# Performance work log

Hardware: AMD Instinct MI355X
Metric: run time of the kernel (lower is better)

The kernel has to match this reference:

```python
import jax, jax.numpy as jnp
import numpy as np

OUT, IN, GROUP = 8192, 8192, 128  # meta.shape=(out,in), group_size over out dim


def unpack_int4(packed, out_shape):
    """Unpack uint8 bytes (two nibbles each) into signed int8 in [-8,7].
    Matches torch: inter[0::2]=lo, inter[1::2]=hi."""
    flat = packed.reshape(-1)
    lo = (flat & 15).astype(jnp.int8)
    hi = ((flat >> 4) & 15).astype(jnp.int8)
    lo = jnp.where(lo >= 8, lo - 16, lo)
    hi = jnp.where(hi >= 8, hi - 16, hi)
    inter = jnp.stack([lo, hi], axis=-1).reshape(-1)  # interleave lo/hi
    total = out_shape[0] * out_shape[1]
    return inter[:total].reshape(out_shape)


def setup_inputs() -> dict:
    key = jax.random.key(0)
    kx, kq, ks, kb = jax.random.split(key, 4)
    x = jax.random.normal(kx, (16, IN), dtype=jnp.float32)
    # packed int4 weights: one byte holds two nibbles -> OUT*IN/2 bytes
    q_packed = jax.random.randint(kq, (OUT * IN // 2,), 0, 256, dtype=jnp.int32).astype(jnp.uint8)
    # per-group scales (group over out dim), positive small values
    scale = jax.random.uniform(ks, (OUT // GROUP,), dtype=jnp.float32) * 0.01 + 1e-4
    bias = jax.random.normal(kb, (OUT,), dtype=jnp.float32) * 0.01
    return {"x": x, "q_packed": q_packed, "scale": scale, "bias": bias}


def reference(x, q_packed, scale, bias):
    # unpack + per-group dequant, then matmul (CPU fallback path of QuantLinear.forward)
    q_int = unpack_int4(q_packed, (OUT, IN)).astype(jnp.float32)  # (OUT, IN)
    s = jnp.repeat(scale, GROUP)[:, None]                         # (OUT, 1) expanded scales
    W = s * q_int                                                 # dequantized fp weight
    return x @ W.T + bias                                         # (B, OUT)
```

## Files before the change

kernel.cpp:

```cpp
#include <hip/hip_runtime.h>
#include <hip/hip_bf16.h>

#define OUT_N 8192
#define IN_N  8192
#define QROW  (IN_N / 2)
#define NCH   8
#define CH32  64

typedef __attribute__((ext_vector_type(8))) short short8v;
typedef __attribute__((ext_vector_type(4))) float f32x4;

__device__ __forceinline__ unsigned int bf16pk(float a, float b) {
    __hip_bfloat162 h = __float22bfloat162_rn(make_float2(a, b));
    unsigned int u;
    __builtin_memcpy(&u, &h, 4);
    return u;
}

__device__ __forceinline__ void gld_lds16(const int* gsrc, int* ldst_base) {
    __builtin_amdgcn_global_load_lds(
        (const __attribute__((address_space(1))) void*)gsrc,
        (__attribute__((address_space(3))) void*)ldst_base, 16, 0, 0);
}

__global__ __launch_bounds__(256) void xconv_kernel(
    const float* __restrict__ x, uint4* __restrict__ xb2)
{
    const int tid = blockIdx.x * 256 + threadIdx.x;
    const int l   = tid & 63;
    const int scs = tid >> 6;
    const int s   = scs & 3;
    const int c   = (scs >> 2) & 7;
    const int w   = scs >> 5;
    const int r   = l & 15;
    const int g   = l >> 4;
    const float* src = x + (size_t)r * IN_N + w * 1024 + c * 128 + s * 32 + g * 8;
    float4 a = *(const float4*)src;
    float4 b = *(const float4*)(src + 4);
    uint4 u = { bf16pk(a.x, a.y), bf16pk(a.z, a.w),
                bf16pk(b.x, b.y), bf16pk(b.z, b.w) };
    xb2[tid] = u;
}

__global__ __launch_bounds__(512, 4) void qlin_mfma_kernel(
    const int*   __restrict__ qp,
    const uint4* __restrict__ xb2,
    const float* __restrict__ scale,
    const float* __restrict__ bias,
    float*       __restrict__ out)
{
    __shared__ int   qbuf[8][2][16 * CH32];
    __shared__ float red[8][16][17];

    const int t = threadIdx.x;
    const int w = t >> 6;
    const int l = t & 63;
    const int g = l >> 4;
    const int r = l & 15;
    const int tile = blockIdx.x;
    const int obase = tile * 16;
    const int ph = tile & 7;

    const int* qwbase = qp + (size_t)obase * QROW + w * (QROW / 8);
    const int drow = l >> 4;
    const uint4* xwbase = xb2 + (w << 11) + l;

    f32x4 acc = {0.f, 0.f, 0.f, 0.f};
    uint4 xr[2][4];

    #pragma unroll
    for (int s = 0; s < 4; ++s)
        xr[0][s] = xwbase[ph * 256 + s * 64];
    #pragma unroll
    for (int p = 0; p < 4; ++p) {
        const int row = 4 * p + drow;
        const int j   = (l & 15) ^ (row & 15);
        gld_lds16(qwbase + (size_t)row * QROW + ph * CH32 + j * 4,
                  &qbuf[w][0][p * 256]);
    }

    #pragma unroll
    for (int c0 = 0; c0 < NCH; ++c0) {
        const int cur = c0 & 1;

        if (c0 + 1 < NCH) {
            const int ccn = (c0 + 1 + ph) & 7;
            #pragma unroll
            for (int s = 0; s < 4; ++s)
                xr[cur ^ 1][s] = xwbase[ccn * 256 + s * 64];
            #pragma unroll
            for (int p = 0; p < 4; ++p) {
                const int row = 4 * p + drow;
                const int j   = (l & 15) ^ (row & 15);
                gld_lds16(qwbase + (size_t)row * QROW + ccn * CH32 + j * 4,
                          &qbuf[w][cur ^ 1][p * 256]);
            }
            asm volatile("s_waitcnt vmcnt(8)" ::: "memory");
        } else {
            asm volatile("s_waitcnt vmcnt(0)" ::: "memory");
        }
        __builtin_amdgcn_sched_barrier(0);

        const char* wb = (const char*)qbuf[w][cur];
        #pragma unroll
        for (int s = 0; s < 4; ++s) {
            const int4 q = *(const int4*)(wb + r * 256 + ((((s << 2) + g) ^ r) << 4));
            uint4 ub = {
                bf16pk((float)((q.x << 28) >> 28), (float)((q.x << 24) >> 28)),
                bf16pk((float)((q.y << 28) >> 28), (float)((q.y << 24) >> 28)),
                bf16pk((float)((q.z << 28) >> 28), (float)((q.z << 24) >> 28)),
                bf16pk((float)((q.w << 28) >> 28), (float)((q.w << 24) >> 28))
            };
            short8v bfrag = __builtin_bit_cast(short8v, ub);
            short8v afrag = __builtin_bit_cast(short8v, xr[cur][s]);
            acc = __builtin_amdgcn_mfma_f32_16x16x32_bf16(afrag, bfrag, acc, 0, 0, 0);
        }
    }

    red[w][g * 4 + 0][r] = acc[0];
    red[w][g * 4 + 1][r] = acc[1];
    red[w][g * 4 + 2][r] = acc[2];
    red[w][g * 4 + 3][r] = acc[3];
    __syncthreads();

    if (t < 256) {
        const int b = t >> 4;
        const int o = t & 15;
        const int oc = obase + o;
        float v = 0.f;
        #pragma unroll
        for (int i = 0; i < 8; ++i) v += red[i][b][o];
        out[b * OUT_N + oc] = v * scale[oc >> 7] + bias[oc];
    }
}

extern "C" void kernel_launch(void* const* d_in, const int* in_sizes, int n_in,
                              void* d_out, int out_size, void* d_ws, size_t ws_size,
                              hipStream_t stream) {
    (void)in_sizes; (void)n_in; (void)ws_size; (void)out_size;
    const float* x     = (const float*)d_in[0];
    const int*   qp    = (const int*)d_in[1];
    const float* scale = (const float*)d_in[2];
    const float* bias  = (const float*)d_in[3];
    float*       out   = (float*)d_out;
    uint4*       xb2   = (uint4*)d_ws;

    xconv_kernel<<<dim3(64), dim3(256), 0, stream>>>(x, xb2);
    qlin_mfma_kernel<<<dim3(OUT_N / 16), dim3(512), 0, stream>>>(qp, xb2, scale, bias, out);
}
```

Before: 30.79 us.

## Split block into producer DMA waves and consumer MFMA waves with LDS flags

Restructures the GEMV kernel so four waves only issue global-to-LDS loads of the int4 weight tile in 16 super-chunks, while four other waves dequantize and run MFMA, synchronizing through LDS flag arrays with spin-waits. The x conversion layout is reordered to match the new per-consumer-wave K split. The aim is to keep more weight loads in flight, decoupled from compute. The cost is spin-wait overhead on volatile LDS flags, half the waves doing no math, and a risk of ordering or visibility problems between the producer's DMA completion and the consumers' reads.

Result: slower. 40.14 us (+30.4%).

```diff
diff --git a/kernel.cpp b/kernel.cpp
--- a/kernel.cpp
+++ b/kernel.cpp
@@ -4,8 +4,8 @@
 #define OUT_N 8192
 #define IN_N  8192
 #define QROW  (IN_N / 2)
-#define NCH   8
-#define CH32  64
+#define NSC   16
+#define SC32  256
 
 typedef __attribute__((ext_vector_type(8))) short short8v;
 typedef __attribute__((ext_vector_type(4))) float f32x4;
@@ -23,18 +23,20 @@
         (__attribute__((address_space(3))) void*)ldst_base, 16, 0, 0);
 }
 
+#define SCHED0() __builtin_amdgcn_sched_barrier(0)
+#define CFENCE() asm volatile("" ::: "memory")
+
 __global__ __launch_bounds__(256) void xconv_kernel(
     const float* __restrict__ x, uint4* __restrict__ xb2)
 {
     const int tid = blockIdx.x * 256 + threadIdx.x;
-    const int l   = tid & 63;
-    const int scs = tid >> 6;
-    const int s   = scs & 3;
-    const int c   = (scs >> 2) & 7;
-    const int w   = scs >> 5;
-    const int r   = l & 15;
-    const int g   = l >> 4;
-    const float* src = x + (size_t)r * IN_N + w * 1024 + c * 128 + s * 32 + g * 8;
+    const int l  = tid & 63;
+    const int s  = (tid >> 6) & 3;
+    const int S  = (tid >> 8) & 15;
+    const int cw = tid >> 12;
+    const int r  = l & 15;
+    const int g  = l >> 4;
+    const float* src = x + (size_t)r * IN_N + S * 512 + cw * 128 + s * 32 + g * 8;
     float4 a = *(const float4*)src;
     float4 b = *(const float4*)(src + 4);
     uint4 u = { bf16pk(a.x, a.y), bf16pk(a.z, a.w),
@@ -42,15 +44,17 @@
     xb2[tid] = u;
 }
 
-__global__ __launch_bounds__(512, 4) void qlin_mfma_kernel(
+__global__ __launch_bounds__(512, 4) void qlin_pc_kernel(
     const int*   __restrict__ qp,
     const uint4* __restrict__ xb2,
     const float* __restrict__ scale,
     const float* __restrict__ bias,
     float*       __restrict__ out)
 {
-    __shared__ int   qbuf[8][2][16 * CH32];
-    __shared__ float red[8][16][17];
+    __shared__ int   qbuf[2][16][SC32];
+    __shared__ float red[4][16][17];
+    __shared__ int   psync[NSC][4];
+    __shared__ int   pdone[NSC][4];
 
     const int t = threadIdx.x;
     const int w = t >> 6;
@@ -59,77 +63,90 @@
     const int r = l & 15;
     const int tile = blockIdx.x;
     const int obase = tile * 16;
-    const int ph = tile & 7;
 
-    const int* qwbase = qp + (size_t)obase * QROW + w * (QROW / 8);
-    const int drow = l >> 4;
-    const uint4* xwbase = xb2 + (w << 11) + l;
+    if (t < NSC * 4) { ((int*)psync)[t] = 0; ((int*)pdone)[t] = 0; }
+    __syncthreads();
 
-    f32x4 acc = {0.f, 0.f, 0.f, 0.f};
-    uint4 xr[2][4];
+    if (w < 4) {
+        const int p = w;
+#define PDMA(S_) do { _Pragma("unroll")                                      \
+        for (int i = 0; i < 4; ++i) {                                        \
+            const int R = 4 * p + i;                                         \
+            gld_lds16(qp + (size_t)(obase + R) * QROW + (S_) * SC32          \
+                         + ((l ^ (R & 15)) << 2),                            \
+                      &qbuf[(S_) & 1][R][0]);                                \
+        } } while (0)
 
-    #pragma unroll
-    for (int s = 0; s < 4; ++s)
-        xr[0][s] = xwbase[ph * 256 + s * 64];
-    #pragma unroll
-    for (int p = 0; p < 4; ++p) {
-        const int row = 4 * p + drow;
-        const int j   = (l & 15) ^ (row & 15);
-        gld_lds16(qwbase + (size_t)row * QROW + ph * CH32 + j * 4,
-                  &qbuf[w][0][p * 256]);
+        PDMA(0);
+        PDMA(1);
+        #pragma unroll
+        for (int S = 0; S < NSC; ++S) {
+            if (S + 1 < NSC) asm volatile("s_waitcnt vmcnt(4)" ::: "memory");
+            else             asm volatile("s_waitcnt vmcnt(0)" ::: "memory");
+            SCHED0();
+            if (l == 0) psync[S][p] = 1;
+            if (S + 2 < NSC) {
+                volatile int* dn = &pdone[S][0];
+                while ((dn[0] & dn[1] & dn[2] & dn[3]) == 0)
+                    asm volatile("s_sleep 1");
+                CFENCE(); SCHED0();
+                PDMA(S + 2);
+            }
+        }
+#undef PDMA
+    } else {
+        const int cw = w - 4;
+        f32x4 acc = {0.f, 0.f, 0.f, 0.f};
+        const uint4* xbase = xb2 + cw * 4096 + l;
+
+        #pragma unroll
+        for (int S = 0; S < NSC; ++S) {
+            uint4 xr0 = xbase[S * 256 +   0];
+            uint4 xr1 = xbase[S * 256 +  64];
+            uint4 xr2 = xbase[S * 256 + 128];
+            uint4 xr3 = xbase[S * 256 + 192];
+            volatile int* sy = &psync[S][0];
+            while ((sy[0] & sy[1] & sy[2] & sy[3]) == 0)
+                asm volatile("s_sleep 1");
+            CFENCE(); SCHED0();
+            asm volatile("s_waitcnt vmcnt(0)" ::: "memory");
+            SCHED0();
+
+            const char* wb = (const char*)&qbuf[S & 1][0][0];
+            #pragma unroll
+            for (int s = 0; s < 4; ++s) {
+                const int slot = cw * 16 + s * 4 + g;
+                const int4 q = *(const int4*)(wb + r * 1024
+                                              + ((slot ^ (r & 15)) << 4));
+                uint4 ub = {
+                    bf16pk((float)((q.x << 28) >> 28), (float)((q.x << 24) >> 28)),
+                    bf16pk((float)((q.y << 28) >> 28), (float)((q.y << 24) >> 28)),
+                    bf16pk((float)((q.z << 28) >> 28), (float)((q.z << 24) >> 28)),
+                    bf16pk((float)((q.w << 28) >> 28), (float)((q.w << 24) >> 28))
+                };
+                short8v bfrag = __builtin_bit_cast(short8v, ub);
+                uint4 xcur = (s == 0) ? xr0 : (s == 1) ? xr1 : (s == 2) ? xr2 : xr3;
+                short8v afrag = __builtin_bit_cast(short8v, xcur);
+                acc = __builtin_amdgcn_mfma_f32_16x16x32_bf16(afrag, bfrag, acc, 0, 0, 0);
+            }
+            asm volatile("s_waitcnt lgkmcnt(0)" ::: "memory");
+            SCHED0();
+            if (l == 0) pdone[S][cw] = 1;
+        }
+
+        red[cw][g * 4 + 0][r] = acc[0];
+        red[cw][g * 4 + 1][r] = acc[1];
+        red[cw][g * 4 + 2][r] = acc[2];
+        red[cw][g * 4 + 3][r] = acc[3];
     }
 
-    #pragma unroll
-    for (int c0 = 0; c0 < NCH; ++c0) {
-        const int cur = c0 & 1;
-
-        if (c0 + 1 < NCH) {
-            const int ccn = (c0 + 1 + ph) & 7;
-            #pragma unroll
-            for (int s = 0; s < 4; ++s)
-                xr[cur ^ 1][s] = xwbase[ccn * 256 + s * 64];
-            #pragma unroll
-            for (int p = 0; p < 4; ++p) {
-                const int row = 4 * p + drow;
-                const int j   = (l & 15) ^ (row & 15);
-                gld_lds16(qwbase + (size_t)row * QROW + ccn * CH32 + j * 4,
-                          &qbuf[w][cur ^ 1][p * 256]);
-            }
-            asm volatile("s_waitcnt vmcnt(8)" ::: "memory");
-        } else {
-            asm volatile("s_waitcnt vmcnt(0)" ::: "memory");
-        }
-        __builtin_amdgcn_sched_barrier(0);
-
-        const char* wb = (const char*)qbuf[w][cur];
-        #pragma unroll
-        for (int s = 0; s < 4; ++s) {
-            const int4 q = *(const int4*)(wb + r * 256 + ((((s << 2) + g) ^ r) << 4));
-            uint4 ub = {
-                bf16pk((float)((q.x << 28) >> 28), (float)((q.x << 24) >> 28)),
-                bf16pk((float)((q.y << 28) >> 28), (float)((q.y << 24) >> 28)),
-                bf16pk((float)((q.z << 28) >> 28), (float)((q.z << 24) >> 28)),
-                bf16pk((float)((q.w << 28) >> 28), (float)((q.w << 24) >> 28))
-            };
-            short8v bfrag = __builtin_bit_cast(short8v, ub);
-            short8v afrag = __builtin_bit_cast(short8v, xr[cur][s]);
-            acc = __builtin_amdgcn_mfma_f32_16x16x32_bf16(afrag, bfrag, acc, 0, 0, 0);
-        }
-    }
-
-    red[w][g * 4 + 0][r] = acc[0];
-    red[w][g * 4 + 1][r] = acc[1];
-    red[w][g * 4 + 2][r] = acc[2];
-    red[w][g * 4 + 3][r] = acc[3];
     __syncthreads();
 
     if (t < 256) {
         const int b = t >> 4;
         const int o = t & 15;
         const int oc = obase + o;
-        float v = 0.f;
-        #pragma unroll
-        for (int i = 0; i < 8; ++i) v += red[i][b][o];
+        float v = red[0][b][o] + red[1][b][o] + red[2][b][o] + red[3][b][o];
         out[b * OUT_N + oc] = v * scale[oc >> 7] + bias[oc];
     }
 }
@@ -146,5 +163,5 @@
     uint4*       xb2   = (uint4*)d_ws;
 
     xconv_kernel<<<dim3(64), dim3(256), 0, stream>>>(x, xb2);
-    qlin_mfma_kernel<<<dim3(OUT_N / 16), dim3(512), 0, stream>>>(qp, xb2, scale, bias, out);
+    qlin_pc_kernel<<<dim3(OUT_N / 16), dim3(512), 0, stream>>>(qp, xb2, scale, bias, out);
 }
```

## Replace direct global-to-LDS loads with register-staged loads and deeper prefetch

Applied to the files above, without the earlier changes.

Weight chunks are now loaded from global memory into registers and then written to LDS by the threads, instead of using the global_load_lds direct path. The pipeline is restructured to prefetch two chunks ahead, storing the next chunk to LDS after the current MFMA work. The aim is to keep more memory requests in flight and overlap them with compute. The cost is more registers, extra LDS write instructions, and fragile hand-tuned vmcnt waits that have to match the new load ordering.

Measured after the change: 57.05 us. +85.3%, slower.

```diff
diff --git a/kernel.cpp b/kernel.cpp
--- a/kernel.cpp
+++ b/kernel.cpp
@@ -17,11 +17,7 @@
     return u;
 }
 
-__device__ __forceinline__ void gld_lds16(const int* gsrc, int* ldst_base) {
-    __builtin_amdgcn_global_load_lds(
-        (const __attribute__((address_space(1))) void*)gsrc,
-        (__attribute__((address_space(3))) void*)ldst_base, 16, 0, 0);
-}
+#define SCHED0() __builtin_amdgcn_sched_barrier(0)
 
 __global__ __launch_bounds__(256) void xconv_kernel(
     const float* __restrict__ x, uint4* __restrict__ xb2)
@@ -66,40 +62,40 @@
     const uint4* xwbase = xb2 + (w << 11) + l;
 
     f32x4 acc = {0.f, 0.f, 0.f, 0.f};
+    int4  qr[2][4];
     uint4 xr[2][4];
 
-    #pragma unroll
-    for (int s = 0; s < 4; ++s)
-        xr[0][s] = xwbase[ph * 256 + s * 64];
-    #pragma unroll
-    for (int p = 0; p < 4; ++p) {
-        const int row = 4 * p + drow;
-        const int j   = (l & 15) ^ (row & 15);
-        gld_lds16(qwbase + (size_t)row * QROW + ph * CH32 + j * 4,
-                  &qbuf[w][0][p * 256]);
+#define QLD(c_, b_) do { _Pragma("unroll")                                    \
+    for (int p = 0; p < 4; ++p) {                                             \
+        const int row = 4 * p + drow;                                         \
+        qr[b_][p] = *(const int4*)(qwbase + (size_t)row * QROW + (c_) * CH32  \
+                                   + (((l & 15) ^ (row & 15)) << 2));         \
+    } } while (0)
+#define XLD(c_, b_) do { _Pragma("unroll")                                    \
+    for (int s = 0; s < 4; ++s) xr[b_][s] = xwbase[(c_) * 256 + s * 64];      \
+    } while (0)
+#define QST(b_) do { _Pragma("unroll")                                        \
+    for (int p = 0; p < 4; ++p)                                               \
+        *(int4*)&qbuf[w][b_][p * 256 + l * 4] = qr[b_][p];                    \
+    } while (0)
+
+    QLD(ph, 0); XLD(ph, 0);
+    asm volatile("s_waitcnt vmcnt(0)" ::: "memory");
+    SCHED0();
+    QST(0);
+    {
+        const int c1 = (1 + ph) & 7;
+        QLD(c1, 1); XLD(c1, 1);
     }
 
     #pragma unroll
     for (int c0 = 0; c0 < NCH; ++c0) {
         const int cur = c0 & 1;
 
-        if (c0 + 1 < NCH) {
-            const int ccn = (c0 + 1 + ph) & 7;
-            #pragma unroll
-            for (int s = 0; s < 4; ++s)
-                xr[cur ^ 1][s] = xwbase[ccn * 256 + s * 64];
-            #pragma unroll
-            for (int p = 0; p < 4; ++p) {
-                const int row = 4 * p + drow;
-                const int j   = (l & 15) ^ (row & 15);
-                gld_lds16(qwbase + (size_t)row * QROW + ccn * CH32 + j * 4,
-                          &qbuf[w][cur ^ 1][p * 256]);
-            }
-            asm volatile("s_waitcnt vmcnt(8)" ::: "memory");
-        } else {
-            asm volatile("s_waitcnt vmcnt(0)" ::: "memory");
-        }
-        __builtin_amdgcn_sched_barrier(0);
+        if (c0 < NCH - 1) asm volatile("s_waitcnt vmcnt(8)" ::: "memory");
+        else              asm volatile("s_waitcnt vmcnt(0)" ::: "memory");
+        asm volatile("s_waitcnt lgkmcnt(0)" ::: "memory");
+        SCHED0();
 
         const char* wb = (const char*)qbuf[w][cur];
         #pragma unroll
@@ -115,7 +111,21 @@
             short8v afrag = __builtin_bit_cast(short8v, xr[cur][s]);
             acc = __builtin_amdgcn_mfma_f32_16x16x32_bf16(afrag, bfrag, acc, 0, 0, 0);
         }
+
+        if (c0 + 1 < NCH) {
+            SCHED0();
+            asm volatile("s_waitcnt vmcnt(4)" ::: "memory");
+            SCHED0();
+            QST(cur ^ 1);
+            if (c0 + 2 < NCH) {
+                const int cc2 = (c0 + 2 + ph) & 7;
+                QLD(cc2, cur); XLD(cc2, cur);
+            }
+        }
     }
+#undef QLD
+#undef XLD
+#undef QST
 
     red[w][g * 4 + 0][r] = acc[0];
     red[w][g * 4 + 1][r] = acc[1];
```
